# Kernel optimization log

Hardware: AMD Instinct MI355X
Metric: run time of the kernel (lower is better)

The kernel has to match this reference:

```python
import jax, jax.numpy as jnp
import numpy as np

DIM = 1024
HEADS = 16
HEAD_DIM = DIM // HEADS
B, N = 8, 1024


def setup_inputs() -> dict:
    key = jax.random.key(0)
    ks = jax.random.split(key, 10)
    s = lambda fan_in: 1.0 / np.sqrt(fan_in)
    return {
        "x": jax.random.normal(ks[0], (B, N, DIM), jnp.float32),
        "pose_angles": jax.random.normal(ks[1], (B, 3), jnp.float32),
        # weights stored (in, out) so y = x @ W + b (equivalent to torch Linear)
        "Wqkv": jax.random.normal(ks[2], (DIM, 3 * DIM), jnp.float32) * s(DIM),
        "bqkv": jnp.zeros((3 * DIM,), jnp.float32),
        "W1": jax.random.normal(ks[3], (3, 64), jnp.float32) * s(3),
        "b1": jnp.zeros((64,), jnp.float32),
        "W2": jax.random.normal(ks[4], (64, 3 * DIM), jnp.float32) * s(64),
        "b2": jnp.zeros((3 * DIM,), jnp.float32),
        "Wproj": jax.random.normal(ks[5], (DIM, DIM), jnp.float32) * s(DIM),
        "bproj": jnp.zeros((DIM,), jnp.float32),
    }


def reference(x, pose_angles, Wqkv, bqkv, W1, b1, W2, b2, Wproj, bproj):
    Bq, Nq, C = x.shape
    H, D = HEADS, HEAD_DIM
    # qkv projection -> [B,N,3,H,D] -> [3,B,H,N,D]
    qkv = (x @ Wqkv + bqkv).reshape(Bq, Nq, 3, H, D).transpose(2, 0, 3, 1, 4)
    q, k, v = qkv[0], qkv[1], qkv[2]
    # pose MLP: 3 -> 64 -> 3*dim, chunked into per-head biases [B,H,1,D]
    pose_emb = jax.nn.relu(pose_angles @ W1 + b1) @ W2 + b2
    pose_q, pose_k, pose_v = jnp.split(pose_emb, 3, axis=1)
    pose_q = pose_q.reshape(Bq, H, 1, D)
    pose_k = pose_k.reshape(Bq, H, 1, D)
    pose_v = pose_v.reshape(Bq, H, 1, D)
    q = q + pose_q
    k = k + pose_k
    v = v + pose_v
    scale = 1.0 / jnp.sqrt(jnp.asarray(D, x.dtype))
    attn = jax.nn.softmax(jnp.einsum("bhnd,bhmd->bhnm", q, k) * scale, axis=-1)
    # dropout is identity in eval mode
    out = jnp.einsum("bhnm,bhmd->bhnd", attn, v)
    out = out.transpose(0, 2, 1, 3).reshape(Bq, Nq, C)
    return out @ Wproj + bproj
```

## Files before the change

kernel.cpp:

```cpp
#include <hip/hip_runtime.h>
#include <stdint.h>

typedef unsigned short u16;
typedef short bf16x8 __attribute__((ext_vector_type(8)));
typedef short bf16x4 __attribute__((ext_vector_type(4)));
typedef float f32x4 __attribute__((ext_vector_type(4)));
typedef u16 u16x4 __attribute__((ext_vector_type(4)));

__device__ __forceinline__ u16 f2bf(float f) {
  union { float f; unsigned int u; } v; v.f = f;
  unsigned int r = v.u + 0x7fffu + ((v.u >> 16) & 1u);
  return (u16)(r >> 16);
}

__device__ __forceinline__ void async16(const void* g, void* l) {
  __builtin_amdgcn_global_load_lds(
      (const __attribute__((address_space(1))) unsigned int*)g,
      (__attribute__((address_space(3))) unsigned int*)l, 16, 0, 0);
}

__device__ __forceinline__ f32x4 mfma16x16(bf16x4 a, bf16x4 b, f32x4 c) {
#if __has_builtin(__builtin_amdgcn_mfma_f32_16x16x16bf16_1k)
  return __builtin_amdgcn_mfma_f32_16x16x16bf16_1k(a, b, c, 0, 0, 0);
#else
  asm volatile("v_mfma_f32_16x16x16_bf16 %0, %1, %2, %0\n\ts_nop 7\n\ts_nop 7"
               : "+v"(c) : "v"(a), "v"(b));
  return c;
#endif
}

__global__ void pose_mlp_kernel(const float* __restrict__ ang, const float* __restrict__ W1,
                                const float* __restrict__ b1, const float* __restrict__ W2,
                                const float* __restrict__ b2, float* __restrict__ pose) {
  __shared__ float hid[8][64];
  int t = threadIdx.x;
  for (int idx = t; idx < 512; idx += 256) {
    int b = idx >> 6, j = idx & 63;
    float a = b1[j];
#pragma unroll
    for (int i = 0; i < 3; ++i) a += ang[b * 3 + i] * W1[i * 64 + j];
    hid[b][j] = fmaxf(a, 0.f);
  }
  __syncthreads();
  int idx = blockIdx.x * 256 + t;
  int b = idx / 3072, c = idx - b * 3072;
  float a = b2[c];
#pragma unroll
  for (int j = 0; j < 64; ++j) a += hid[b][j] * W2[j * 3072 + c];
  pose[idx] = a;
}

__global__ void cast_x_kernel(const float4* __restrict__ x, u16x4* __restrict__ y, int n4) {
  int i = blockIdx.x * blockDim.x + threadIdx.x;
  const int stride = gridDim.x * blockDim.x;
  for (; i < n4; i += stride) {
    float4 v = x[i];
    u16x4 o;
    o[0] = f2bf(v.x); o[1] = f2bf(v.y); o[2] = f2bf(v.z); o[3] = f2bf(v.w);
    y[i] = o;
  }
}

__global__ void transpose_cast_kernel(const float* __restrict__ W, u16* __restrict__ Wt,
                                      int Kdim, int Ncol) {
  __shared__ float tile[64][65];
  const int tx = threadIdx.x, ty = threadIdx.y;
  const int c0 = blockIdx.x * 64, k0 = blockIdx.y * 64;
#pragma unroll
  for (int rr = 0; rr < 16; ++rr) {
    int row = rr * 4 + ty;
    tile[row][tx] = W[(size_t)(k0 + row) * Ncol + c0 + tx];
  }
  __syncthreads();
#pragma unroll
  for (int rr = 0; rr < 16; ++rr) {
    int row = rr * 4 + ty;
    Wt[(size_t)(c0 + row) * Kdim + k0 + tx] = f2bf(tile[tx][row]);
  }
}

template <int EPI>
__global__ void __launch_bounds__(256) gemm_bt_kernel(
    const u16* __restrict__ A, const u16* __restrict__ Bt,
    const float* __restrict__ bias, const float* __restrict__ pose,
    u16* __restrict__ qout, u16* __restrict__ kout, u16* __restrict__ vtout,
    float* __restrict__ cout, int Kdim, int Ncols) {
  __shared__ u16 ldsA[128 * 64];
  __shared__ u16 ldsB[128 * 64];
  const int t = threadIdx.x, l = t & 63, w = t >> 6;
  const int g = l >> 4, r16 = l & 15;
  const int wr = w >> 1, wc = w & 1;
  const int n0 = blockIdx.x * 128, m0 = blockIdx.y * 128;
  const u16* Ab = A + (size_t)m0 * Kdim;
  const u16* Bb = Bt + (size_t)n0 * Kdim;
  f32x4 acc[4][4] = {};
  for (int kt = 0; kt < Kdim; kt += 64) {
#pragma unroll
    for (int ii = 0; ii < 4; ++ii) {
      int idx = ii * 256 + t, row = idx >> 3, seg = idx & 7;
      async16(Ab + (size_t)row * Kdim + kt + seg * 8, &ldsA[(ii * 256 + w * 64) * 8]);
    }
#pragma unroll
    for (int ii = 0; ii < 4; ++ii) {
      int idx = ii * 256 + t, row = idx >> 3, seg = idx & 7;
      async16(Bb + (size_t)row * Kdim + kt + seg * 8, &ldsB[(ii * 256 + w * 64) * 8]);
    }
    __syncthreads();
#pragma unroll
    for (int ks = 0; ks < 2; ++ks) {
      bf16x8 a[4], bb[4];
#pragma unroll
      for (int i = 0; i < 4; ++i)
        a[i] = *(const bf16x8*)&ldsA[(wr * 64 + i * 16 + r16) * 64 + ks * 32 + g * 8];
#pragma unroll
      for (int j = 0; j < 4; ++j)
        bb[j] = *(const bf16x8*)&ldsB[(wc * 64 + j * 16 + r16) * 64 + ks * 32 + g * 8];
#pragma unroll
      for (int i = 0; i < 4; ++i)
#pragma unroll
        for (int j = 0; j < 4; ++j)
          acc[i][j] = __builtin_amdgcn_mfma_f32_16x16x32_bf16(a[i], bb[j], acc[i][j], 0, 0, 0);
    }
    __syncthreads();
  }
#pragma unroll
  for (int i = 0; i < 4; ++i)
#pragma unroll
    for (int j = 0; j < 4; ++j)
#pragma unroll
      for (int r = 0; r < 4; ++r) {
        int row = m0 + wr * 64 + i * 16 + g * 4 + r;
        int col = n0 + wc * 64 + j * 16 + r16;
        float v = acc[i][j][r] + bias[col];
        if (EPI == 0) {
          int b = row >> 10, n = row & 1023;
          v += pose[b * 3072 + col];
          u16 hv = f2bf(v);
          int three = col >> 10, hh = (col >> 6) & 15, d = col & 63;
          size_t bhh = (size_t)(b * 16 + hh);
          if (three == 0)      qout[(bhh * 1024 + n) * 64 + d] = hv;
          else if (three == 1) kout[(bhh * 1024 + n) * 64 + d] = hv;
          else                 vtout[(bhh * 64 + d) * 1024 + n] = hv;
        } else {
          cout[(size_t)row * Ncols + col] = v;
        }
      }
}

__global__ void __launch_bounds__(256) attn_kernel(
    const u16* __restrict__ Qb, const u16* __restrict__ Kb,
    const u16* __restrict__ Vtb, u16* __restrict__ aout) {
  __shared__ u16 ldsK[64][72];
  __shared__ u16 ldsV[64][72];
  const int t = threadIdx.x, l = t & 63, w = t >> 6;
  const int g = l >> 4, r16 = l & 15;
  const int bh = blockIdx.x >> 4, qt = blockIdx.x & 15;
  const int b = bh >> 4, h = bh & 15;
  const int q0 = qt * 64 + w * 16;
  const u16* Qp = Qb + ((size_t)bh * 1024 + q0 + r16) * 64;
  bf16x8 qreg0 = *(const bf16x8*)(Qp + g * 8);
  bf16x8 qreg1 = *(const bf16x8*)(Qp + 32 + g * 8);
  const u16* Kbase = Kb + (size_t)bh * 1024 * 64;
  const u16* Vbase = Vtb + (size_t)bh * 64 * 1024;
  float m = -1e30f, rs = 0.f;
  f32x4 o[4] = {};
  for (int key0 = 0; key0 < 1024; key0 += 64) {
#pragma unroll
    for (int ii = 0; ii < 2; ++ii) {
      int idx = ii * 256 + t, row = idx >> 3, seg = idx & 7;
      *(bf16x8*)&ldsK[row][seg * 8] = *(const bf16x8*)(Kbase + (size_t)(key0 + row) * 64 + seg * 8);
      *(bf16x8*)&ldsV[row][seg * 8] = *(const bf16x8*)(Vbase + (size_t)row * 1024 + key0 + seg * 8);
    }
    __syncthreads();
    f32x4 s[4] = {};
#pragma unroll
    for (int f = 0; f < 4; ++f) {
      bf16x8 ak0 = *(const bf16x8*)&ldsK[f * 16 + r16][g * 8];
      s[f] = __builtin_amdgcn_mfma_f32_16x16x32_bf16(ak0, qreg0, s[f], 0, 0, 0);
      bf16x8 ak1 = *(const bf16x8*)&ldsK[f * 16 + r16][32 + g * 8];
      s[f] = __builtin_amdgcn_mfma_f32_16x16x32_bf16(ak1, qreg1, s[f], 0, 0, 0);
    }
    float mt = -1e30f;
#pragma unroll
    for (int f = 0; f < 4; ++f)
#pragma unroll
      for (int r = 0; r < 4; ++r) { s[f][r] *= 0.125f; mt = fmaxf(mt, s[f][r]); }
    mt = fmaxf(mt, __shfl_xor(mt, 16));
    mt = fmaxf(mt, __shfl_xor(mt, 32));
    float mnew = fmaxf(m, mt);
    float alpha = __expf(m - mnew);
    float rt = 0.f;
    bf16x4 pa[4];
#pragma unroll
    for (int f = 0; f < 4; ++f) {
#pragma unroll
      for (int r = 0; r < 4; ++r) {
        float p = __expf(s[f][r] - mnew);
        rt += p;
        pa[f][r] = (short)f2bf(p);
      }
    }
    rt += __shfl_xor(rt, 16);
    rt += __shfl_xor(rt, 32);
    rs = rs * alpha + rt;
    m = mnew;
    float ar[4];
#pragma unroll
    for (int r = 0; r < 4; ++r) ar[r] = __shfl(alpha, (l & 48) | (g * 4 + r));
#pragma unroll
    for (int nf = 0; nf < 4; ++nf)
#pragma unroll
      for (int r = 0; r < 4; ++r) o[nf][r] *= ar[r];
#pragma unroll
    for (int s4 = 0; s4 < 4; ++s4)
#pragma unroll
      for (int nf = 0; nf < 4; ++nf) {
        bf16x4 bv = *(const bf16x4*)&ldsV[nf * 16 + r16][s4 * 16 + g * 4];
        o[nf] = mfma16x16(pa[s4], bv, o[nf]);
      }
    __syncthreads();
  }
  float rr[4];
#pragma unroll
  for (int r = 0; r < 4; ++r) rr[r] = __shfl(1.0f / rs, (l & 48) | (g * 4 + r));
#pragma unroll
  for (int nf = 0; nf < 4; ++nf)
#pragma unroll
    for (int r = 0; r < 4; ++r) {
      int qq = qt * 64 + w * 16 + g * 4 + r;
      int d = nf * 16 + r16;
      aout[((size_t)b * 1024 + qq) * 1024 + h * 64 + d] = f2bf(o[nf][r] * rr[r]);
    }
}

extern "C" void kernel_launch(void* const* d_in, const int* in_sizes, int n_in,
                              void* d_out, int out_size, void* d_ws, size_t ws_size,
                              hipStream_t stream) {
  (void)in_sizes; (void)n_in; (void)out_size; (void)ws_size;
  const float* x     = (const float*)d_in[0];
  const float* ang   = (const float*)d_in[1];
  const float* Wqkv  = (const float*)d_in[2];
  const float* bqkv  = (const float*)d_in[3];
  const float* W1    = (const float*)d_in[4];
  const float* b1    = (const float*)d_in[5];
  const float* W2    = (const float*)d_in[6];
  const float* b2    = (const float*)d_in[7];
  const float* Wproj = (const float*)d_in[8];
  const float* bproj = (const float*)d_in[9];
  float* out = (float*)d_out;
  char* ws = (char*)d_ws;

  u16* xh     = (u16*)(ws);
  u16* wqkvt  = (u16*)(ws + (size_t)16 * 1024 * 1024);
  u16* wprojt = (u16*)(ws + (size_t)22 * 1024 * 1024);
  float* pose = (float*)(ws + (size_t)24 * 1024 * 1024);
  u16* Qb     = (u16*)(ws + (size_t)25 * 1024 * 1024);
  u16* Kb     = (u16*)(ws + (size_t)41 * 1024 * 1024);
  u16* Vtb    = (u16*)(ws + (size_t)57 * 1024 * 1024);

  pose_mlp_kernel<<<96, 256, 0, stream>>>(ang, W1, b1, W2, b2, pose);
  cast_x_kernel<<<2048, 256, 0, stream>>>((const float4*)x, (u16x4*)xh, 8 * 1024 * 1024 / 4);
  transpose_cast_kernel<<<dim3(48, 16), dim3(64, 4), 0, stream>>>(Wqkv, wqkvt, 1024, 3072);
  transpose_cast_kernel<<<dim3(16, 16), dim3(64, 4), 0, stream>>>(Wproj, wprojt, 1024, 1024);
  gemm_bt_kernel<0><<<dim3(24, 64), 256, 0, stream>>>(xh, wqkvt, bqkv, pose,
                                                      Qb, Kb, Vtb, nullptr, 1024, 3072);
  attn_kernel<<<2048, 256, 0, stream>>>(Qb, Kb, Vtb, xh);
  gemm_bt_kernel<1><<<dim3(8, 64), 256, 0, stream>>>(xh, wprojt, bproj, nullptr,
                                                     nullptr, nullptr, nullptr, out, 1024, 1024);
}
```

Measured before the change: 237.1 us.

## Double-buffer GEMM LDS tiles and swizzle block order across XCDs

The bf16 GEMM kernel now uses two LDS buffers per operand, so the async global-to-LDS loads for the next K tile are issued before the MFMA work on the current tile, replacing the two-barrier-per-iteration serial load/compute loop. The launch grid becomes 1D, and block indices are remapped so that consecutive tiles land on the same XCD (grid divided into 8 chunks), which is meant to improve L2 reuse of the A/B rows. LDS use doubles to 64KB per block, which may reduce occupancy, and the remap assumes the grid size is divisible by 8.

New measurement: 228.6 us. 1.04x faster.

```diff
diff --git a/kernel.cpp b/kernel.cpp
--- a/kernel.cpp
+++ b/kernel.cpp
@@ -84,44 +84,57 @@
     const u16* __restrict__ A, const u16* __restrict__ Bt,
     const float* __restrict__ bias, const float* __restrict__ pose,
     u16* __restrict__ qout, u16* __restrict__ kout, u16* __restrict__ vtout,
-    float* __restrict__ cout, int Kdim, int Ncols) {
-  __shared__ u16 ldsA[128 * 64];
-  __shared__ u16 ldsB[128 * 64];
+    float* __restrict__ cout, int Kdim, int Ncols, int nTilesX) {
+  __shared__ u16 ldsA[2][128 * 64];
+  __shared__ u16 ldsB[2][128 * 64];
   const int t = threadIdx.x, l = t & 63, w = t >> 6;
   const int g = l >> 4, r16 = l & 15;
   const int wr = w >> 1, wc = w & 1;
-  const int n0 = blockIdx.x * 128, m0 = blockIdx.y * 128;
+  const int nwg = gridDim.x, cpx = nwg >> 3;
+  const int swz = (blockIdx.x & 7) * cpx + (blockIdx.x >> 3);
+  const int n0 = (swz % nTilesX) * 128, m0 = (swz / nTilesX) * 128;
   const u16* Ab = A + (size_t)m0 * Kdim;
   const u16* Bb = Bt + (size_t)n0 * Kdim;
-  f32x4 acc[4][4] = {};
-  for (int kt = 0; kt < Kdim; kt += 64) {
+
+  auto stage = [&](int buf, int kt) {
 #pragma unroll
     for (int ii = 0; ii < 4; ++ii) {
       int idx = ii * 256 + t, row = idx >> 3, seg = idx & 7;
-      async16(Ab + (size_t)row * Kdim + kt + seg * 8, &ldsA[(ii * 256 + w * 64) * 8]);
+      async16(Ab + (size_t)row * Kdim + kt + seg * 8, &ldsA[buf][(ii * 256 + w * 64) * 8]);
     }
 #pragma unroll
     for (int ii = 0; ii < 4; ++ii) {
       int idx = ii * 256 + t, row = idx >> 3, seg = idx & 7;
-      async16(Bb + (size_t)row * Kdim + kt + seg * 8, &ldsB[(ii * 256 + w * 64) * 8]);
-    }
-    __syncthreads();
+      async16(Bb + (size_t)row * Kdim + kt + seg * 8, &ldsB[buf][(ii * 256 + w * 64) * 8]);
+    }
+  };
+
+  f32x4 acc[4][4] = {};
+  const int nIter = Kdim >> 6;
+  stage(0, 0);
+  asm volatile("s_waitcnt vmcnt(0)" ::: "memory");
+  __builtin_amdgcn_s_barrier();
+  int cur = 0;
+  for (int it = 0; it < nIter; ++it) {
+    if (it + 1 < nIter) stage(cur ^ 1, (it + 1) << 6);
 #pragma unroll
     for (int ks = 0; ks < 2; ++ks) {
       bf16x8 a[4], bb[4];
 #pragma unroll
       for (int i = 0; i < 4; ++i)
-        a[i] = *(const bf16x8*)&ldsA[(wr * 64 + i * 16 + r16) * 64 + ks * 32 + g * 8];
+        a[i] = *(const bf16x8*)&ldsA[cur][(wr * 64 + i * 16 + r16) * 64 + ks * 32 + g * 8];
 #pragma unroll
       for (int j = 0; j < 4; ++j)
-        bb[j] = *(const bf16x8*)&ldsB[(wc * 64 + j * 16 + r16) * 64 + ks * 32 + g * 8];
+        bb[j] = *(const bf16x8*)&ldsB[cur][(wc * 64 + j * 16 + r16) * 64 + ks * 32 + g * 8];
 #pragma unroll
       for (int i = 0; i < 4; ++i)
 #pragma unroll
         for (int j = 0; j < 4; ++j)
           acc[i][j] = __builtin_amdgcn_mfma_f32_16x16x32_bf16(a[i], bb[j], acc[i][j], 0, 0, 0);
     }
-    __syncthreads();
+    asm volatile("s_waitcnt vmcnt(0)" ::: "memory");
+    __builtin_amdgcn_s_barrier();
+    cur ^= 1;
   }
 #pragma unroll
   for (int i = 0; i < 4; ++i)
@@ -262,9 +275,9 @@
   cast_x_kernel<<<2048, 256, 0, stream>>>((const float4*)x, (u16x4*)xh, 8 * 1024 * 1024 / 4);
   transpose_cast_kernel<<<dim3(48, 16), dim3(64, 4), 0, stream>>>(Wqkv, wqkvt, 1024, 3072);
   transpose_cast_kernel<<<dim3(16, 16), dim3(64, 4), 0, stream>>>(Wproj, wprojt, 1024, 1024);
-  gemm_bt_kernel<0><<<dim3(24, 64), 256, 0, stream>>>(xh, wqkvt, bqkv, pose,
-                                                      Qb, Kb, Vtb, nullptr, 1024, 3072);
+  gemm_bt_kernel<0><<<1536, 256, 0, stream>>>(xh, wqkvt, bqkv, pose,
+                                              Qb, Kb, Vtb, nullptr, 1024, 3072, 24);
   attn_kernel<<<2048, 256, 0, stream>>>(Qb, Kb, Vtb, xh);
-  gemm_bt_kernel<1><<<dim3(8, 64), 256, 0, stream>>>(xh, wprojt, bproj, nullptr,
-                                                     nullptr, nullptr, nullptr, out, 1024, 1024);
-}
+  gemm_bt_kernel<1><<<512, 256, 0, stream>>>(xh, wprojt, bproj, nullptr,
+                                             nullptr, nullptr, nullptr, out, 1024, 1024, 8);
+}
```
